# Kernel tuning notes

Measured on AMD Instinct MI355X. Metric: run time of the kernel, lower is better.

Reference implementation:

```python
import jax, jax.numpy as jnp
import numpy as np

D_MODEL = 1024
N_HEADS = 16
D_K = D_MODEL // N_HEADS
SCALE = float(np.sqrt(D_K))


def setup_inputs() -> dict:
    key = jax.random.key(0)
    ks = jax.random.split(key, 8)
    B, S = 2, 2048
    std = 1.0 / np.sqrt(D_MODEL)
    return {
        "query": jax.random.normal(ks[0], (B, S, D_MODEL), dtype=jnp.float32),
        "key": jax.random.normal(ks[1], (B, S, D_MODEL), dtype=jnp.float32),
        "value": jax.random.normal(ks[2], (B, S, D_MODEL), dtype=jnp.float32),
        "w_q": jax.random.normal(ks[3], (D_MODEL, D_MODEL), dtype=jnp.float32) * std,
        "w_k": jax.random.normal(ks[4], (D_MODEL, D_MODEL), dtype=jnp.float32) * std,
        "w_v": jax.random.normal(ks[5], (D_MODEL, D_MODEL), dtype=jnp.float32) * std,
        "w_o": jax.random.normal(ks[6], (D_MODEL, D_MODEL), dtype=jnp.float32) * std,
        "b_o": jax.random.normal(ks[7], (D_MODEL,), dtype=jnp.float32) * std,
    }


def reference(query, key, value, w_q, w_k, w_v, w_o, b_o):
    B, S, _ = query.shape
    # torch nn.Linear: y = x @ W^T
    def proj(x, w):
        # [B,S,D] -> [B,H,S,d_k]
        y = jnp.einsum("bsd,ed->bse", x, w)
        return y.reshape(B, S, N_HEADS, D_K).transpose(0, 2, 1, 3)

    Q = proj(query, w_q)
    K = proj(key, w_k)
    V = proj(value, w_v)
    scores = jnp.einsum("bhqd,bhkd->bhqk", Q, K) / SCALE  # [B,H,S,S]
    attn = jax.nn.softmax(scores, axis=-1)
    # dropout is identity in eval mode
    ctx = jnp.einsum("bhqk,bhkd->bhqd", attn, V)  # [B,H,S,d_k]
    ctx = ctx.transpose(0, 2, 1, 3).reshape(B, S, D_MODEL)
    out = jnp.einsum("bsd,ed->bse", ctx, w_o) + b_o
    return out, attn
```

## Files before the change

kernel.cpp:

```cpp
#include <hip/hip_runtime.h>
#include <cstdint>
#include <cstddef>

#define SEQ   2048
#define NH    16
#define DKD   64
#define DM    1024

typedef __attribute__((ext_vector_type(8))) short bf16x8;
typedef __attribute__((ext_vector_type(4))) short bf16x4;
typedef __attribute__((ext_vector_type(4))) float f32x4;
typedef unsigned short u16;

__device__ __forceinline__ u16 f2bf(float f) {
    union { float f; unsigned u; } v; v.f = f;
    unsigned r = v.u + 0x7fff + ((v.u >> 16) & 1);
    return (u16)(r >> 16);
}
__device__ __forceinline__ float bf2f(u16 b) {
    union { unsigned u; float f; } v; v.u = ((unsigned)b) << 16;
    return v.f;
}
__device__ __forceinline__ float exp2_hw(float x) { return __builtin_amdgcn_exp2f(x); }
__device__ __forceinline__ float log2_hw(float x) { return __builtin_amdgcn_logf(x); }

__device__ __forceinline__ void gload16(const void* g, void* l) {
    __builtin_amdgcn_global_load_lds(
        (const __attribute__((address_space(1))) void*)g,
        (__attribute__((address_space(3))) void*)l, 16, 0, 0);
}

__global__ __launch_bounds__(256)
void cast_all(const float* __restrict__ q, const float* __restrict__ k,
              const float* __restrict__ v, const float* __restrict__ wq,
              const float* __restrict__ wk, const float* __restrict__ wv,
              const float* __restrict__ wo,
              u16* __restrict__ qb, u16* __restrict__ kb, u16* __restrict__ vb,
              u16* __restrict__ wb) {
    const int z = blockIdx.y;
    const float* s;
    u16* d;
    if (z < 12) {
        int a = z >> 2;
        s = (a == 0 ? q : a == 1 ? k : v) + (size_t)(z & 3) * 1048576;
        d = (a == 0 ? qb : a == 1 ? kb : vb) + (size_t)(z & 3) * 1048576;
    } else {
        int a = z - 12;
        s = (a == 0 ? wq : a == 1 ? wk : a == 2 ? wv : wo);
        d = wb + (size_t)a * 1048576;
    }
    size_t i = ((size_t)blockIdx.x * 256 + threadIdx.x) * 8;
    f32x4 x0 = *(const f32x4*)&s[i];
    f32x4 x1 = *(const f32x4*)&s[i + 4];
    bf16x8 o;
#pragma unroll
    for (int j = 0; j < 4; j++) { o[j] = (short)f2bf(x0[j]); o[j + 4] = (short)f2bf(x1[j]); }
    *(bf16x8*)&d[i] = o;
}

__global__ __launch_bounds__(256, 3)
void qkv_gemm(const u16* __restrict__ qb, const u16* __restrict__ kb,
              const u16* __restrict__ vb, const u16* __restrict__ wb,
              u16* __restrict__ Qw, u16* __restrict__ Kw, u16* __restrict__ Vtw) {
    __shared__ u16 As[128][64];
    __shared__ u16 Bs[128][64];

    const int hwid = blockIdx.x + 8 * blockIdx.y + 256 * blockIdx.z;
    const int lgc  = (hwid & 7) * 96 + (hwid >> 3);
    const int z    = lgc >> 8;
    const int m0   = ((lgc >> 3) & 31) * 128;
    const int n0   = (lgc & 7) * 128;

    const u16* A  = (z == 0) ? qb : (z == 1) ? kb : vb;
    const u16* Bm = wb + (size_t)z * 1048576;
    u16*      dst = (z == 0) ? Qw : (z == 1) ? Kw : Vtw;
    const float sc = (z == 0) ? 0.125f * 1.44269504088896f : 1.0f;

    const int t    = threadIdx.x;
    const int w    = t >> 6;
    const int ln   = t & 63;
    const int l16  = ln & 15;
    const int quad = ln >> 4;
    const int wr   = (w >> 1) * 64;
    const int wc   = (w & 1) * 64;
    const int sr   = ln >> 3;
    const int sc8  = (ln & 7) * 8;

    f32x4 acc[4][4];
#pragma unroll
    for (int i = 0; i < 4; i++)
#pragma unroll
        for (int j = 0; j < 4; j++) {
            f32x4 zz = {0.f, 0.f, 0.f, 0.f};
            acc[i][j] = zz;
        }

    for (int k0 = 0; k0 < 1024; k0 += 64) {
#pragma unroll
        for (int i = 0; i < 4; i++) {
            int chunk = w * 4 + i;
            int r = chunk * 8 + sr;
            gload16(&A [(size_t)(m0 + r) * 1024 + k0 + sc8], &As[chunk * 8][0]);
            gload16(&Bm[(size_t)(n0 + r) * 1024 + k0 + sc8], &Bs[chunk * 8][0]);
        }
        __syncthreads();
#pragma unroll
        for (int ks = 0; ks < 2; ks++) {
            bf16x8 af[4], bfr[4];
#pragma unroll
            for (int i = 0; i < 4; i++)
                af[i] = *(const bf16x8*)&As[wr + i * 16 + l16][ks * 32 + quad * 8];
#pragma unroll
            for (int j = 0; j < 4; j++)
                bfr[j] = *(const bf16x8*)&Bs[wc + j * 16 + l16][ks * 32 + quad * 8];
#pragma unroll
            for (int i = 0; i < 4; i++)
#pragma unroll
                for (int j = 0; j < 4; j++)
                    acc[i][j] = __builtin_amdgcn_mfma_f32_16x16x32_bf16(
                        af[i], bfr[j], acc[i][j], 0, 0, 0);
        }
        __syncthreads();
    }

#pragma unroll
    for (int i = 0; i < 4; i++)
#pragma unroll
        for (int j = 0; j < 4; j++)
#pragma unroll
            for (int r = 0; r < 4; r++) {
                int row = m0 + wr + i * 16 + quad * 4 + r;
                int col = n0 + wc + j * 16 + l16;
                float val = acc[i][j][r] * sc;
                int b = row >> 11, s = row & 2047, h = col >> 6, dk = col & 63;
                if (z < 2)
                    dst[((size_t)((b * 16 + h) * 2048 + s)) * 64 + dk] = f2bf(val);
                else
                    dst[((size_t)((b * 16 + h) * 64 + dk)) * 2048 + s] = f2bf(val);
            }
}

__global__ __launch_bounds__(256, 3)
void out_gemm(const u16* __restrict__ A, const u16* __restrict__ Bm,
              float* __restrict__ dst, const float* __restrict__ bias) {
    __shared__ u16 As[128][64];
    __shared__ u16 Bs[64][64];

    const int hwid = blockIdx.x + 16 * blockIdx.y;
    const int lgc  = (hwid & 7) * 64 + (hwid >> 3);
    const int m0   = (lgc >> 4) * 128;
    const int n0   = (lgc & 15) * 64;

    const int t    = threadIdx.x;
    const int w    = t >> 6;
    const int ln   = t & 63;
    const int l16  = ln & 15;
    const int quad = ln >> 4;
    const int wr   = (w >> 1) * 64;
    const int wc   = (w & 1) * 32;
    const int sr   = ln >> 3;
    const int sc8  = (ln & 7) * 8;

    f32x4 acc[4][2];
#pragma unroll
    for (int i = 0; i < 4; i++)
#pragma unroll
        for (int j = 0; j < 2; j++) {
            f32x4 zz = {0.f, 0.f, 0.f, 0.f};
            acc[i][j] = zz;
        }

    for (int k0 = 0; k0 < 1024; k0 += 64) {
#pragma unroll
        for (int i = 0; i < 4; i++) {
            int chunk = w * 4 + i;
            int r = chunk * 8 + sr;
            gload16(&A[(size_t)(m0 + r) * 1024 + k0 + sc8], &As[chunk * 8][0]);
        }
#pragma unroll
        for (int i = 0; i < 2; i++) {
            int chunk = w * 2 + i;
            int r = chunk * 8 + sr;
            gload16(&Bm[(size_t)(n0 + r) * 1024 + k0 + sc8], &Bs[chunk * 8][0]);
        }
        __syncthreads();
#pragma unroll
        for (int ks = 0; ks < 2; ks++) {
            bf16x8 af[4], bfr[2];
#pragma unroll
            for (int i = 0; i < 4; i++)
                af[i] = *(const bf16x8*)&As[wr + i * 16 + l16][ks * 32 + quad * 8];
#pragma unroll
            for (int j = 0; j < 2; j++)
                bfr[j] = *(const bf16x8*)&Bs[wc + j * 16 + l16][ks * 32 + quad * 8];
#pragma unroll
            for (int i = 0; i < 4; i++)
#pragma unroll
                for (int j = 0; j < 2; j++)
                    acc[i][j] = __builtin_amdgcn_mfma_f32_16x16x32_bf16(
                        af[i], bfr[j], acc[i][j], 0, 0, 0);
        }
        __syncthreads();
    }

#pragma unroll
    for (int i = 0; i < 4; i++)
#pragma unroll
        for (int j = 0; j < 2; j++)
#pragma unroll
            for (int r = 0; r < 4; r++) {
                int row = m0 + wr + i * 16 + quad * 4 + r;
                int col = n0 + wc + j * 16 + l16;
                dst[(size_t)row * 1024 + col] = acc[i][j][r] + bias[col];
            }
}

__global__ __launch_bounds__(512, 4)
void attn_kernel(const u16* __restrict__ Qw, const u16* __restrict__ Kw,
                 const u16* __restrict__ Vtw,
                 float* __restrict__ attn_out, u16* __restrict__ ctx_out) {
    __shared__ u16 H[2][128][72];
    __shared__ u16 Ps[128][136];
    u16 (*Vts)[136] = (u16(*)[136])&H[1][0][0];

    const int t    = threadIdx.x;
    const int hwid = blockIdx.x + 16 * blockIdx.y;
    const int lgc  = (hwid & 7) * 64 + (hwid >> 3);
    const int bh   = lgc >> 4;
    const int q0   = (lgc & 15) * 128;
    const int w    = t >> 6;
    const int lane = t & 63;
    const int l16  = lane & 15;
    const int quad = lane >> 4;

    const u16* Qh = Qw  + (size_t)bh * SEQ * DKD;
    const u16* Kh = Kw  + (size_t)bh * SEQ * DKD;
    const u16* Vh = Vtw + (size_t)bh * DKD * SEQ;

    bf16x8 qf[2];
#pragma unroll
    for (int ks = 0; ks < 2; ks++)
        qf[ks] = *(const bf16x8*)&Qh[(size_t)(q0 + w * 16 + l16) * 64 + ks * 32 + quad * 8];

    const int kr0 = t >> 3,         kc0 = (t & 7) * 8;
    const int kr1 = (t + 512) >> 3, kc1 = ((t + 512) & 7) * 8;
    const int vr0 = t >> 4,         vc0 = (t & 15) * 8;
    const int vr1 = (t + 512) >> 4, vc1 = ((t + 512) & 15) * 8;

    float lsum[4];
#pragma unroll
    for (int r = 0; r < 4; r++) lsum[r] = 0.f;

    bf16x8 kp0 = *(const bf16x8*)&Kh[(size_t)kr0 * 64 + kc0];
    bf16x8 kp1 = *(const bf16x8*)&Kh[(size_t)kr1 * 64 + kc1];
    for (int kt = 0; kt < 16; kt++) {
        u16 (*KA)[72] = H[kt & 1];
        *(bf16x8*)&KA[kr0][kc0] = kp0;
        *(bf16x8*)&KA[kr1][kc1] = kp1;
        if (kt < 15) {
            kp0 = *(const bf16x8*)&Kh[(size_t)((kt + 1) * 128 + kr0) * 64 + kc0];
            kp1 = *(const bf16x8*)&Kh[(size_t)((kt + 1) * 128 + kr1) * 64 + kc1];
        }
        __syncthreads();

        f32x4 s[8];
#pragma unroll
        for (int j = 0; j < 8; j++) { f32x4 zz = {0.f,0.f,0.f,0.f}; s[j] = zz; }
        __builtin_amdgcn_s_setprio(1);
#pragma unroll
        for (int ks = 0; ks < 2; ks++)
#pragma unroll
            for (int j = 0; j < 8; j++) {
                bf16x8 b = *(const bf16x8*)&KA[j * 16 + l16][ks * 32 + quad * 8];
                s[j] = __builtin_amdgcn_mfma_f32_16x16x32_bf16(qf[ks], b, s[j], 0, 0, 0);
            }
        __builtin_amdgcn_s_setprio(0);
#pragma unroll
        for (int j = 0; j < 8; j++)
#pragma unroll
            for (int r = 0; r < 4; r++)
                lsum[r] += exp2_hw(s[j][r]);
    }

    float lnl2[4];
#pragma unroll
    for (int r = 0; r < 4; r++) {
#pragma unroll
        for (int d = 1; d < 16; d <<= 1) lsum[r] += __shfl_xor(lsum[r], d, 64);
        lnl2[r] = log2_hw(lsum[r]);
    }

    f32x4 o[4];
#pragma unroll
    for (int jo = 0; jo < 4; jo++) { f32x4 zz = {0.f,0.f,0.f,0.f}; o[jo] = zz; }

    kp0 = *(const bf16x8*)&Kh[(size_t)kr0 * 64 + kc0];
    kp1 = *(const bf16x8*)&Kh[(size_t)kr1 * 64 + kc1];
    bf16x8 vp0 = *(const bf16x8*)&Vh[(size_t)vr0 * 2048 + vc0];
    bf16x8 vp1 = *(const bf16x8*)&Vh[(size_t)vr1 * 2048 + vc1];
    for (int kt = 0; kt < 16; kt++) {
        __syncthreads();
        *(bf16x8*)&H[0][kr0][kc0] = kp0;
        *(bf16x8*)&H[0][kr1][kc1] = kp1;
        *(bf16x8*)&Vts[vr0][vc0]  = vp0;
        *(bf16x8*)&Vts[vr1][vc1]  = vp1;
        if (kt < 15) {
            kp0 = *(const bf16x8*)&Kh[(size_t)((kt + 1) * 128 + kr0) * 64 + kc0];
            kp1 = *(const bf16x8*)&Kh[(size_t)((kt + 1) * 128 + kr1) * 64 + kc1];
            vp0 = *(const bf16x8*)&Vh[(size_t)vr0 * 2048 + (kt + 1) * 128 + vc0];
            vp1 = *(const bf16x8*)&Vh[(size_t)vr1 * 2048 + (kt + 1) * 128 + vc1];
        }
        __syncthreads();

        f32x4 s[8];
#pragma unroll
        for (int j = 0; j < 8; j++) { f32x4 zz = {0.f,0.f,0.f,0.f}; s[j] = zz; }
        __builtin_amdgcn_s_setprio(1);
#pragma unroll
        for (int ks = 0; ks < 2; ks++)
#pragma unroll
            for (int j = 0; j < 8; j++) {
                bf16x8 b = *(const bf16x8*)&H[0][j * 16 + l16][ks * 32 + quad * 8];
                s[j] = __builtin_amdgcn_mfma_f32_16x16x32_bf16(qf[ks], b, s[j], 0, 0, 0);
            }
        __builtin_amdgcn_s_setprio(0);

#pragma unroll
        for (int j = 0; j < 8; j++)
#pragma unroll
            for (int r = 0; r < 4; r++) {
                float p = exp2_hw(s[j][r] - lnl2[r]);
                Ps[w * 16 + quad * 4 + r][j * 16 + l16] = f2bf(p);
            }

        bf16x8 pa[4];
#pragma unroll
        for (int ks = 0; ks < 4; ks++)
            pa[ks] = *(const bf16x8*)&Ps[w * 16 + l16][ks * 32 + quad * 8];
        __builtin_amdgcn_s_setprio(1);
#pragma unroll
        for (int jo = 0; jo < 4; jo++)
#pragma unroll
            for (int ks = 0; ks < 4; ks++) {
                bf16x8 vb = *(const bf16x8*)&Vts[jo * 16 + l16][ks * 32 + quad * 8];
                o[jo] = __builtin_amdgcn_mfma_f32_16x16x32_bf16(pa[ks], vb, o[jo], 0, 0, 0);
            }
        __builtin_amdgcn_s_setprio(0);

#pragma unroll
        for (int i = 0; i < 8; i++) {
            int cw = lane + 64 * i;
            int r  = cw >> 5;
            int c4 = (cw & 31) * 4;
            bf16x4 pv = *(const bf16x4*)&Ps[w * 16 + r][c4];
            f32x4 o4;
#pragma unroll
            for (int j = 0; j < 4; j++) o4[j] = bf2f((u16)pv[j]);
            __builtin_nontemporal_store(o4,
                (f32x4*)&attn_out[((size_t)(bh * 2048 + q0 + w * 16 + r)) * 2048 + kt * 128 + c4]);
        }
    }

    const int b = bh >> 4, h = bh & 15;
#pragma unroll
    for (int jo = 0; jo < 4; jo++)
#pragma unroll
        for (int r = 0; r < 4; r++) {
            int srow = q0 + w * 16 + quad * 4 + r;
            int dcol = h * 64 + jo * 16 + l16;
            ctx_out[((size_t)(b * 2048 + srow)) * 1024 + dcol] = f2bf(o[jo][r]);
        }
}

extern "C" void kernel_launch(void* const* d_in, const int* in_sizes, int n_in,
                              void* d_out, int out_size, void* d_ws, size_t ws_size,
                              hipStream_t stream) {
    (void)in_sizes; (void)n_in; (void)out_size; (void)ws_size;

    const float* q  = (const float*)d_in[0];
    const float* k  = (const float*)d_in[1];
    const float* v  = (const float*)d_in[2];
    const float* wq = (const float*)d_in[3];
    const float* wk = (const float*)d_in[4];
    const float* wv = (const float*)d_in[5];
    const float* wo = (const float*)d_in[6];
    const float* bo = (const float*)d_in[7];

    float* out  = (float*)d_out;
    float* attn = out + (size_t)4194304;

    u16* Qw   = (u16*)d_ws;
    u16* Kw   = Qw   + (size_t)4194304;
    u16* Vtw  = Kw   + (size_t)4194304;
    u16* ctxb = Vtw  + (size_t)4194304;
    u16* qb   = ctxb + (size_t)4194304;
    u16* kb   = qb   + (size_t)4194304;
    u16* vb   = kb   + (size_t)4194304;
    u16* wb   = vb   + (size_t)4194304;

    dim3 blk(256);
    cast_all<<<dim3(512, 16), blk, 0, stream>>>(q, k, v, wq, wk, wv, wo,
                                                qb, kb, vb, wb);
    qkv_gemm<<<dim3(8, 32, 3), blk, 0, stream>>>(qb, kb, vb, wb, Qw, Kw, Vtw);
    attn_kernel<<<dim3(16, 32), dim3(512), 0, stream>>>(Qw, Kw, Vtw, attn, ctxb);
    out_gemm<<<dim3(16, 32), blk, 0, stream>>>(ctxb, wb + (size_t)3 * 1048576, out, bo);
}
```

Baseline: 699.3 us.

## Load V fragments directly from global and double-buffer K tiles

The PV pass no longer stages V through shared memory. Each wave now loads its V^T MFMA operand fragments straight from global memory into registers, issuing them in two halves so the loads overlap the QK MFMAs. The K tile alternates between the two shared-memory buffers, which removes the leading __syncthreads per iteration. The cost is that every wave re-reads the whole V tile, multiplying global/L2 traffic for V, and holds 64 extra VGPRs, which may hurt occupancy or cause spills under the launch bounds.

```diff
diff --git a/kernel.cpp b/kernel.cpp
--- a/kernel.cpp
+++ b/kernel.cpp
@@ -221,7 +221,6 @@
                  float* __restrict__ attn_out, u16* __restrict__ ctx_out) {
     __shared__ u16 H[2][128][72];
     __shared__ u16 Ps[128][136];
-    u16 (*Vts)[136] = (u16(*)[136])&H[1][0][0];
 
     const int t    = threadIdx.x;
     const int hwid = blockIdx.x + 16 * blockIdx.y;
@@ -244,8 +243,7 @@
 
     const int kr0 = t >> 3,         kc0 = (t & 7) * 8;
     const int kr1 = (t + 512) >> 3, kc1 = ((t + 512) & 7) * 8;
-    const int vr0 = t >> 4,         vc0 = (t & 15) * 8;
-    const int vr1 = (t + 512) >> 4, vc1 = ((t + 512) & 15) * 8;
+    const u16* Vb = Vh + (size_t)l16 * 2048 + quad * 8;
 
     float lsum[4];
 #pragma unroll
@@ -296,19 +294,19 @@
 
     kp0 = *(const bf16x8*)&Kh[(size_t)kr0 * 64 + kc0];
     kp1 = *(const bf16x8*)&Kh[(size_t)kr1 * 64 + kc1];
-    bf16x8 vp0 = *(const bf16x8*)&Vh[(size_t)vr0 * 2048 + vc0];
-    bf16x8 vp1 = *(const bf16x8*)&Vh[(size_t)vr1 * 2048 + vc1];
     for (int kt = 0; kt < 16; kt++) {
-        __syncthreads();
-        *(bf16x8*)&H[0][kr0][kc0] = kp0;
-        *(bf16x8*)&H[0][kr1][kc1] = kp1;
-        *(bf16x8*)&Vts[vr0][vc0]  = vp0;
-        *(bf16x8*)&Vts[vr1][vc1]  = vp1;
+        u16 (*KA)[72] = H[kt & 1];
+        *(bf16x8*)&KA[kr0][kc0] = kp0;
+        *(bf16x8*)&KA[kr1][kc1] = kp1;
+        bf16x8 vf0[2][4];
+#pragma unroll
+        for (int jo = 0; jo < 2; jo++)
+#pragma unroll
+            for (int ks = 0; ks < 4; ks++)
+                vf0[jo][ks] = *(const bf16x8*)(Vb + (size_t)jo * 32768 + kt * 128 + ks * 32);
         if (kt < 15) {
             kp0 = *(const bf16x8*)&Kh[(size_t)((kt + 1) * 128 + kr0) * 64 + kc0];
             kp1 = *(const bf16x8*)&Kh[(size_t)((kt + 1) * 128 + kr1) * 64 + kc1];
-            vp0 = *(const bf16x8*)&Vh[(size_t)vr0 * 2048 + (kt + 1) * 128 + vc0];
-            vp1 = *(const bf16x8*)&Vh[(size_t)vr1 * 2048 + (kt + 1) * 128 + vc1];
         }
         __syncthreads();
 
@@ -320,10 +318,17 @@
         for (int ks = 0; ks < 2; ks++)
 #pragma unroll
             for (int j = 0; j < 8; j++) {
-                bf16x8 b = *(const bf16x8*)&H[0][j * 16 + l16][ks * 32 + quad * 8];
+                bf16x8 b = *(const bf16x8*)&KA[j * 16 + l16][ks * 32 + quad * 8];
                 s[j] = __builtin_amdgcn_mfma_f32_16x16x32_bf16(qf[ks], b, s[j], 0, 0, 0);
             }
         __builtin_amdgcn_s_setprio(0);
+
+        bf16x8 vf1[2][4];
+#pragma unroll
+        for (int jo = 0; jo < 2; jo++)
+#pragma unroll
+            for (int ks = 0; ks < 4; ks++)
+                vf1[jo][ks] = *(const bf16x8*)(Vb + (size_t)(jo + 2) * 32768 + kt * 128 + ks * 32);
 
 #pragma unroll
         for (int j = 0; j < 8; j++)
@@ -339,12 +344,15 @@
             pa[ks] = *(const bf16x8*)&Ps[w * 16 + l16][ks * 32 + quad * 8];
         __builtin_amdgcn_s_setprio(1);
 #pragma unroll
-        for (int jo = 0; jo < 4; jo++)
-#pragma unroll
-            for (int ks = 0; ks < 4; ks++) {
-                bf16x8 vb = *(const bf16x8*)&Vts[jo * 16 + l16][ks * 32 + quad * 8];
-                o[jo] = __builtin_amdgcn_mfma_f32_16x16x32_bf16(pa[ks], vb, o[jo], 0, 0, 0);
-            }
+        for (int jo = 0; jo < 2; jo++)
+#pragma unroll
+            for (int ks = 0; ks < 4; ks++)
+                o[jo] = __builtin_amdgcn_mfma_f32_16x16x32_bf16(pa[ks], vf0[jo][ks], o[jo], 0, 0, 0);
+#pragma unroll
+        for (int jo = 0; jo < 2; jo++)
+#pragma unroll
+            for (int ks = 0; ks < 4; ks++)
+                o[jo + 2] = __builtin_amdgcn_mfma_f32_16x16x32_bf16(pa[ks], vf1[jo][ks], o[jo + 2], 0, 0, 0);
         __builtin_amdgcn_s_setprio(0);
 
 #pragma unroll
```

Measured after the change: 844.4 us. 1.21x slower.
